# Performance work log

Hardware: AMD Instinct MI355X
Metric: run time of the kernel (lower is better)

The kernel has to match this reference:

```python
import jax, jax.numpy as jnp
import numpy as np

THRESHOLD = 0.0025
EPS = 1e-12
NORM_EPS = 1e-12  # torch F.normalize default eps


def _l2n(x):
    # F.normalize(x, p=2, dim=1): x / max(||x||_2, eps)
    n = jnp.sqrt(jnp.sum(x * x, axis=1, keepdims=True))
    return x / jnp.maximum(n, NORM_EPS)


def _memory_unit(feature, memory):
    # feature: [N, C], memory: [M, C]
    nf = _l2n(feature)
    nm = _l2n(memory)
    w = jax.nn.softmax(nf @ nm.T, axis=1)            # [N, M] cosine sims -> softmax
    # hard_shrink: relu(w - t) * w / (|w - t| + eps)
    w = jax.nn.relu(w - THRESHOLD) * w / (jnp.abs(w - THRESHOLD) + EPS)
    # L1 normalize rows
    w = w / jnp.maximum(jnp.sum(jnp.abs(w), axis=1, keepdims=True), NORM_EPS)
    mf = w @ memory                                   # [N, C] memory read
    return mf, w


def setup_inputs() -> dict:
    key = jax.random.key(0)
    ks = jax.random.split(key, 6)
    N, M = 16384, 1024
    chans = [256, 512, 1024]
    d = {}
    for i, c in enumerate(chans):
        d[f"feat{i}"] = jax.random.normal(ks[i], (N, c), dtype=jnp.float32)
        d[f"mem{i}"] = jax.random.normal(ks[3 + i], (M, c), dtype=jnp.float32)
    return d


def reference(feat0, feat1, feat2, mem0, mem1, mem2):
    outs = []
    weights = []
    for f, m in ((feat0, mem0), (feat1, mem1), (feat2, mem2)):
        mf, w = _memory_unit(f, m)
        outs.append(jnp.concatenate((mf, f), axis=1))  # cat along channel dim
        weights.append(w)
    return (outs[0], outs[1], outs[2], weights[0], weights[1], weights[2])
```

## Files before the change

### kernel.cpp

```cpp
#include <hip/hip_runtime.h>
#include <stdint.h>

typedef float f32x4 __attribute__((ext_vector_type(4)));
typedef short s16x8 __attribute__((ext_vector_type(8)));
typedef short s16x4 __attribute__((ext_vector_type(4)));

__device__ __forceinline__ unsigned short f2bf(float f) {
    uint32_t u = __float_as_uint(f);
    u += 0x7FFFu + ((u >> 16) & 1u);
    return (unsigned short)(u >> 16);
}

__device__ __forceinline__ void g2l16(const short* g, short* l) {
    __builtin_amdgcn_global_load_lds(
        (const __attribute__((address_space(1))) uint32_t*)g,
        (__attribute__((address_space(3))) uint32_t*)l, 16, 0, 0);
}

template<int C>
__device__ __forceinline__ void prep_body(const float* __restrict__ mp,
                                          short* __restrict__ nmp,
                                          int ct, short* stage) {
    const int tid = threadIdx.x;
    const int row = tid >> 4;
    const int c4  = tid & 15;
    constexpr int IT = C / 64;
    const f32x4* src = (const f32x4*)(mp + (size_t)(ct * 16 + row) * C);
    f32x4 vals[IT];
    float ss = 0.f;
#pragma unroll
    for (int i = 0; i < IT; ++i) {
        f32x4 v = src[c4 + 16 * i];
        vals[i] = v;
        ss += v.x * v.x + v.y * v.y + v.z * v.z + v.w * v.w;
    }
#pragma unroll
    for (int m = 1; m < 16; m <<= 1) ss += __shfl_xor(ss, m);
    const float inv = 1.f / fmaxf(sqrtf(ss), 1e-12f);
#pragma unroll
    for (int i = 0; i < IT; ++i) {
        f32x4 v = vals[i];
        s16x4 o;
        o[0] = (short)f2bf(v.x * inv);
        o[1] = (short)f2bf(v.y * inv);
        o[2] = (short)f2bf(v.z * inv);
        o[3] = (short)f2bf(v.w * inv);
        *(s16x4*)&stage[row * C + (c4 + 16 * i) * 4] = o;
    }
    __syncthreads();
    const int lane = tid & 63;
    const int wv = tid >> 6;
    constexpr int NKB = C / 32;
#pragma unroll
    for (int j = 0; j < NKB / 4; ++j) {
        const int kb = j * 4 + wv;
        const s16x8 v = *(const s16x8*)&stage[(lane & 15) * C + kb * 32 + (lane >> 4) * 8];
        *(s16x8*)&nmp[((size_t)ct * NKB + kb) * 512 + lane * 8] = v;
    }
}

__global__ __launch_bounds__(256) void prep_all(const float* m0, short* n0,
                                                const float* m1, short* n1,
                                                const float* m2, short* n2) {
    __shared__ short stage[16 * 1024];
    const int bid = blockIdx.x;
    if (bid < 64) prep_body<256>(m0, n0, bid, stage);
    else if (bid < 128) prep_body<512>(m1, n1, bid - 64, stage);
    else prep_body<1024>(m2, n2, bid - 128, stage);
}

template<int C>
__device__ __forceinline__ void gemm_body(const float* __restrict__ feat,
                                          const float* __restrict__ memv,
                                          const short* __restrict__ nm,
                                          float* __restrict__ out_cat,
                                          float* __restrict__ out_w,
                                          int tile,
                                          short* __restrict__ Bst,
                                          short* __restrict__ As,
                                          float (*__restrict__ red)[64],
                                          float* __restrict__ rowT,
                                          float* __restrict__ rowL,
                                          float* __restrict__ invL,
                                          int* __restrict__ rowflag,
                                          int* __restrict__ anyflag) {
    constexpr int NKB = C / 32;
    constexpr int NCH = C / 64;
    const int tid  = threadIdx.x;
    const int w    = tid >> 6;
    const int lane = tid & 63;
    const int g    = lane >> 4;
    const int ml   = lane & 15;
    const int swz  = ml & 7;
    const int row0 = tile * 64;

    const int frow = tid >> 4;
    const int fk4  = tid & 15;
    const float* fsrc = feat + (size_t)(row0 + frow) * C + fk4 * 4;
    const int ldsW = frow * 64 + (((fk4 >> 1) ^ (frow & 7)) << 3) + (fk4 & 1) * 4;
    const short* nbG = nm + (size_t)(w * 4) * NKB * 512 + lane * 8;
    short* bD0 = Bst + (w * 4) * 512 + lane * 8;
    short* bD1 = Bst + 32768 + (w * 4) * 512 + lane * 8;

    if (tid == 0) *anyflag = 0;

    f32x4 acc[4][4];
#pragma unroll
    for (int r = 0; r < 4; ++r)
#pragma unroll
        for (int ct = 0; ct < 4; ++ct)
            acc[r][ct] = (f32x4){0.f, 0.f, 0.f, 0.f};

    float ss = 0.f;

    const f32x4 v0 = *(const f32x4*)fsrc;
    f32x4 fnxt;
    if (NCH > 1) fnxt = *(const f32x4*)(fsrc + 64);
    __builtin_amdgcn_sched_barrier(0);
#pragma unroll
    for (int p = 0; p < 4; ++p)
        g2l16(nbG + (size_t)p * NKB * 512, bD0 + p * 512);
#pragma unroll
    for (int p = 0; p < 4; ++p)
        g2l16(nbG + ((size_t)p * NKB + 1) * 512, bD1 + p * 512);
    __builtin_amdgcn_sched_barrier(0);
    {
        ss += v0.x * v0.x + v0.y * v0.y + v0.z * v0.z + v0.w * v0.w;
        s16x4 o;
        o[0] = (short)f2bf(v0.x); o[1] = (short)f2bf(v0.y);
        o[2] = (short)f2bf(v0.z); o[3] = (short)f2bf(v0.w);
        *(s16x4*)&As[ldsW] = o;
    }
    asm volatile("s_waitcnt lgkmcnt(0)" ::: "memory");
    __builtin_amdgcn_s_barrier();
    asm volatile("" ::: "memory");

    for (int kb = 0; kb < NKB; ++kb) {
        const int chunk = kb >> 1;
        if ((kb & 1) == 0 && chunk + 1 < NCH) {
            ss += fnxt.x * fnxt.x + fnxt.y * fnxt.y + fnxt.z * fnxt.z + fnxt.w * fnxt.w;
            s16x4 o;
            o[0] = (short)f2bf(fnxt.x); o[1] = (short)f2bf(fnxt.y);
            o[2] = (short)f2bf(fnxt.z); o[3] = (short)f2bf(fnxt.w);
            *(s16x4*)&As[((chunk + 1) & 1) * 4096 + ldsW] = o;
        }
        if (kb == 0 || kb == NKB - 2) asm volatile("s_waitcnt vmcnt(4)" ::: "memory");
        else if (kb == NKB - 1)       asm volatile("s_waitcnt vmcnt(0)" ::: "memory");
        else                          asm volatile("s_waitcnt vmcnt(5)" ::: "memory");
        const short* Bb = Bst + (kb & 1) * 32768 + (w * 4) * 512 + lane * 8;
        s16x8 b[4];
#pragma unroll
        for (int p = 0; p < 4; ++p)
            b[p] = *(const s16x8*)(Bb + p * 512);
        const short* Ab = &As[(chunk & 1) * 4096];
        const int gr = ((kb & 1) << 2) | g;
        s16x8 a[4];
#pragma unroll
        for (int r = 0; r < 4; ++r)
            a[r] = *(const s16x8*)&Ab[(r * 16 + ml) * 64 + ((gr ^ swz) << 3)];
        asm volatile("s_waitcnt lgkmcnt(0)" ::: "memory");
        __builtin_amdgcn_sched_barrier(0);
        if (kb + 2 < NKB) {
            short* bDn = Bst + (kb & 1) * 32768 + (w * 4) * 512 + lane * 8;
#pragma unroll
            for (int p = 0; p < 4; ++p)
                g2l16(nbG + ((size_t)p * NKB + kb + 2) * 512, bDn + p * 512);
        }
        __builtin_amdgcn_sched_barrier(0);
        if ((kb & 1) == 0 && chunk + 2 < NCH)
            fnxt = *(const f32x4*)(fsrc + (size_t)(chunk + 2) * 64);
        __builtin_amdgcn_sched_barrier(0);
        __builtin_amdgcn_s_setprio(1);
#pragma unroll
        for (int r = 0; r < 4; ++r)
#pragma unroll
            for (int ct = 0; ct < 4; ++ct)
                acc[r][ct] = __builtin_amdgcn_mfma_f32_16x16x32_bf16(a[r], b[ct], acc[r][ct], 0, 0, 0);
        __builtin_amdgcn_s_setprio(0);
        if ((kb & 1) == 1 && kb + 1 < NKB) {
            asm volatile("s_waitcnt lgkmcnt(0)" ::: "memory");
            __builtin_amdgcn_s_barrier();
            asm volatile("" ::: "memory");
        }
    }

#pragma unroll
    for (int m = 1; m < 16; m <<= 1) ss += __shfl_xor(ss, m);
    if (fk4 == 0) invL[frow] = 1.f / fmaxf(sqrtf(ss), 1e-12f);
    __syncthreads();

#pragma unroll
    for (int r = 0; r < 4; ++r)
#pragma unroll
        for (int i = 0; i < 4; ++i) {
            const float inv = invL[r * 16 + 4 * g + i];
            float s = 0.f;
#pragma unroll
            for (int ct = 0; ct < 4; ++ct) {
                const float e = __expf(acc[r][ct][i] * inv);
                acc[r][ct][i] = e;
                s += e;
            }
#pragma unroll
            for (int m = 1; m < 16; m <<= 1) s += __shfl_xor(s, m);
            if (ml == 0) red[w][r * 16 + 4 * g + i] = s;
        }
    __syncthreads();
    if (tid < 64) {
        float t = red[0][tid];
#pragma unroll
        for (int ww = 1; ww < 16; ++ww) t += red[ww][tid];
        rowT[tid] = 1.f / t;
    }
    __syncthreads();

#pragma unroll
    for (int r = 0; r < 4; ++r)
#pragma unroll
        for (int i = 0; i < 4; ++i) {
            const float tinv = rowT[r * 16 + 4 * g + i];
            float l1 = 0.f;
#pragma unroll
            for (int ct = 0; ct < 4; ++ct) {
                const float wv = acc[r][ct][i] * tinv;
                const float d = wv - 0.0025f;
                const float v = (d > 0.f) ? (d * wv / (d + 1e-12f)) : 0.f;
                acc[r][ct][i] = v;
                l1 += v;
            }
#pragma unroll
            for (int m = 1; m < 16; m <<= 1) l1 += __shfl_xor(l1, m);
            if (ml == 0) red[w][r * 16 + 4 * g + i] = l1;
        }
    __syncthreads();
    if (tid < 64) {
        float t = red[0][tid];
#pragma unroll
        for (int ww = 1; ww < 16; ++ww) t += red[ww][tid];
        rowL[tid] = 1.f / fmaxf(t, 1e-12f);
        rowflag[tid] = (t > 0.f) ? 1 : 0;
        if (t > 0.f) *anyflag = 1;
    }
    __syncthreads();

#pragma unroll
    for (int r = 0; r < 4; ++r)
#pragma unroll
        for (int i = 0; i < 4; ++i) {
            const float il = rowL[r * 16 + 4 * g + i];
            float* orow = out_w + (size_t)(row0 + r * 16 + 4 * g + i) * 1024;
#pragma unroll
            for (int ct = 0; ct < 4; ++ct)
                orow[(w * 4 + ct) * 16 + ml] = acc[r][ct][i] * il;
        }

    {
        float* fzro = out_cat + (size_t)(row0 + frow) * (2 * C) + fk4 * 4;
        float* fcpy = out_cat + (size_t)(row0 + frow) * (2 * C) + C + fk4 * 4;
        const f32x4 z4 = {0.f, 0.f, 0.f, 0.f};
#pragma unroll
        for (int ch = 0; ch < NCH; ++ch)
            __builtin_nontemporal_store(z4, (f32x4*)(fzro + (size_t)ch * 64));
#pragma unroll
        for (int ch = 0; ch < NCH; ++ch) {
            const f32x4 v = *(const f32x4*)(fsrc + (size_t)ch * 64);
            __builtin_nontemporal_store(v, (f32x4*)(fcpy + (size_t)ch * 64));
        }
    }

    if (*anyflag != 0) {
        __threadfence();
        __syncthreads();
        constexpr int CC = C / 64;
#pragma unroll
        for (int rr = 0; rr < 4; ++rr) {
            const int row = w * 4 + rr;
            if (!rowflag[row]) continue;
            float* dst = out_cat + (size_t)(row0 + row) * (2 * C);
            float mfacc[CC];
#pragma unroll
            for (int cc = 0; cc < CC; ++cc) mfacc[cc] = 0.f;
            const float* wrow = out_w + (size_t)(row0 + row) * 1024;
            for (int jb = 0; jb < 1024; jb += 64) {
                const float wv = wrow[jb + lane];
                unsigned long long msk = __ballot(wv != 0.f);
                while (msk) {
                    const int j = __builtin_ctzll(msk);
                    msk &= msk - 1;
                    const float val = __shfl(wv, j);
                    const float* mrow = memv + (size_t)(jb + j) * C;
#pragma unroll
                    for (int cc = 0; cc < CC; ++cc)
                        mfacc[cc] += val * mrow[cc * 64 + lane];
                }
            }
#pragma unroll
            for (int cc = 0; cc < CC; ++cc) dst[cc * 64 + lane] = mfacc[cc];
        }
    }
}

__global__ __launch_bounds__(1024) void gemm_all(
        const float* f0, const float* m0, const short* n0, float* o0, float* w0,
        const float* f1, const float* m1, const short* n1, float* o1, float* w1,
        const float* f2, const float* m2, const short* n2, float* o2, float* w2) {
    __shared__ short Bst[2 * 32768];
    __shared__ short As[2 * 4096];
    __shared__ float red[16][64];
    __shared__ float rowT[64];
    __shared__ float rowL[64];
    __shared__ float invL[64];
    __shared__ int rowflag[64];
    __shared__ int anyflag;

    const int bid = blockIdx.x;
    if (bid < 256)
        gemm_body<1024>(f2, m2, n2, o2, w2, bid,
                        Bst, As, red, rowT, rowL, invL, rowflag, &anyflag);
    else if (bid < 512)
        gemm_body<512>(f1, m1, n1, o1, w1, bid - 256,
                       Bst, As, red, rowT, rowL, invL, rowflag, &anyflag);
    else
        gemm_body<256>(f0, m0, n0, o0, w0, bid - 512,
                       Bst, As, red, rowT, rowL, invL, rowflag, &anyflag);
}

extern "C" void kernel_launch(void* const* d_in, const int* in_sizes, int n_in,
                              void* d_out, int out_size, void* d_ws, size_t ws_size,
                              hipStream_t stream) {
    const float* feat[3] = {nullptr, nullptr, nullptr};
    const float* memp[3] = {nullptr, nullptr, nullptr};
    for (int i = 0; i < n_in && i < 6; ++i) {
        const int s = in_sizes[i];
        const float* p = (const float*)d_in[i];
        if (s == 16384 * 256) feat[0] = p;
        else if (s == 16384 * 512) feat[1] = p;
        else if (s == 16384 * 1024) feat[2] = p;
        else if (s == 1024 * 256) memp[0] = p;
        else if (s == 1024 * 512) memp[1] = p;
        else if (s == 1024 * 1024) memp[2] = p;
    }
    float* out = (float*)d_out;
    short* nm0 = (short*)d_ws;
    short* nm1 = nm0 + 1024 * 256;
    short* nm2 = nm1 + 1024 * 512;

    const size_t O0 = 0;
    const size_t O1 = (size_t)16384 * 512;
    const size_t O2 = O1 + (size_t)16384 * 1024;
    const size_t W0 = O2 + (size_t)16384 * 2048;
    const size_t W1 = W0 + (size_t)16384 * 1024;
    const size_t W2 = W1 + (size_t)16384 * 1024;

    prep_all<<<192, 256, 0, stream>>>(memp[0], nm0, memp[1], nm1, memp[2], nm2);

    gemm_all<<<768, 1024, 0, stream>>>(
        feat[0], memp[0], nm0, out + O0, out + W0,
        feat[1], memp[1], nm1, out + O1, out + W1,
        feat[2], memp[2], nm2, out + O2, out + W2);
}
```

Baseline: 174.5 us.

## Interleave feature copy and zero-fill stores into the GEMM main loop

Moves the copy of the input features into the concatenated output, and the zero-fill of the memory-feature half, out of the epilogue and into the K-loop. The stores reuse the feature values already loaded for bf16 conversion, so the second global read of the features goes away. The vmcnt wait counts are retuned to account for the extra in-flight stores. This risks mis-synchronisation if the counts are wrong. It also drops the nontemporal hint on these stores.

```diff
diff --git a/kernel.cpp b/kernel.cpp
--- a/kernel.cpp
+++ b/kernel.cpp
@@ -97,6 +97,9 @@
     const int frow = tid >> 4;
     const int fk4  = tid & 15;
     const float* fsrc = feat + (size_t)(row0 + frow) * C + fk4 * 4;
+    float* fcpy = out_cat + (size_t)(row0 + frow) * (2 * C) + C + fk4 * 4;
+    float* fzro = out_cat + (size_t)(row0 + frow) * (2 * C) + fk4 * 4;
+    const f32x4 z4 = {0.f, 0.f, 0.f, 0.f};
     const int ldsW = frow * 64 + (((fk4 >> 1) ^ (frow & 7)) << 3) + (fk4 & 1) * 4;
     const short* nbG = nm + (size_t)(w * 4) * NKB * 512 + lane * 8;
     short* bD0 = Bst + (w * 4) * 512 + lane * 8;
@@ -130,6 +133,7 @@
         o[0] = (short)f2bf(v0.x); o[1] = (short)f2bf(v0.y);
         o[2] = (short)f2bf(v0.z); o[3] = (short)f2bf(v0.w);
         *(s16x4*)&As[ldsW] = o;
+        *(f32x4*)fcpy = v0;
     }
     asm volatile("s_waitcnt lgkmcnt(0)" ::: "memory");
     __builtin_amdgcn_s_barrier();
@@ -137,16 +141,21 @@
 
     for (int kb = 0; kb < NKB; ++kb) {
         const int chunk = kb >> 1;
-        if ((kb & 1) == 0 && chunk + 1 < NCH) {
-            ss += fnxt.x * fnxt.x + fnxt.y * fnxt.y + fnxt.z * fnxt.z + fnxt.w * fnxt.w;
+        f32x4 fold;
+        const bool dofill = ((kb & 1) == 0 && chunk + 1 < NCH);
+        if (dofill) {
+            fold = fnxt;
+            ss += fold.x * fold.x + fold.y * fold.y + fold.z * fold.z + fold.w * fold.w;
             s16x4 o;
-            o[0] = (short)f2bf(fnxt.x); o[1] = (short)f2bf(fnxt.y);
-            o[2] = (short)f2bf(fnxt.z); o[3] = (short)f2bf(fnxt.w);
+            o[0] = (short)f2bf(fold.x); o[1] = (short)f2bf(fold.y);
+            o[2] = (short)f2bf(fold.z); o[3] = (short)f2bf(fold.w);
             *(s16x4*)&As[((chunk + 1) & 1) * 4096 + ldsW] = o;
         }
-        if (kb == 0 || kb == NKB - 2) asm volatile("s_waitcnt vmcnt(4)" ::: "memory");
-        else if (kb == NKB - 1)       asm volatile("s_waitcnt vmcnt(0)" ::: "memory");
-        else                          asm volatile("s_waitcnt vmcnt(5)" ::: "memory");
+        if (kb == 0)                 asm volatile("s_waitcnt vmcnt(5)" ::: "memory");
+        else if (kb == NKB - 1)      asm volatile("s_waitcnt vmcnt(2)" ::: "memory");
+        else if (kb == NKB - 3)      asm volatile("s_waitcnt vmcnt(6)" ::: "memory");
+        else if (kb & 1)             asm volatile("s_waitcnt vmcnt(7)" ::: "memory");
+        else                         asm volatile("s_waitcnt vmcnt(6)" ::: "memory");
         const short* Bb = Bst + (kb & 1) * 32768 + (w * 4) * 512 + lane * 8;
         s16x8 b[4];
 #pragma unroll
@@ -177,6 +186,15 @@
             for (int ct = 0; ct < 4; ++ct)
                 acc[r][ct] = __builtin_amdgcn_mfma_f32_16x16x32_bf16(a[r], b[ct], acc[r][ct], 0, 0, 0);
         __builtin_amdgcn_s_setprio(0);
+        __builtin_amdgcn_sched_barrier(0);
+        if (kb & 1) {
+            *(f32x4*)(fzro + (size_t)chunk * 64) = z4;
+        } else if (dofill) {
+            *(f32x4*)(fcpy + (size_t)(chunk + 1) * 64) = fold;
+        } else {
+            *(f32x4*)(fzro + (size_t)(NCH - 1) * 64) = z4;
+        }
+        __builtin_amdgcn_sched_barrier(0);
         if ((kb & 1) == 1 && kb + 1 < NKB) {
             asm volatile("s_waitcnt lgkmcnt(0)" ::: "memory");
             __builtin_amdgcn_s_barrier();
@@ -253,20 +271,6 @@
             for (int ct = 0; ct < 4; ++ct)
                 orow[(w * 4 + ct) * 16 + ml] = acc[r][ct][i] * il;
         }
-
-    {
-        float* fzro = out_cat + (size_t)(row0 + frow) * (2 * C) + fk4 * 4;
-        float* fcpy = out_cat + (size_t)(row0 + frow) * (2 * C) + C + fk4 * 4;
-        const f32x4 z4 = {0.f, 0.f, 0.f, 0.f};
-#pragma unroll
-        for (int ch = 0; ch < NCH; ++ch)
-            __builtin_nontemporal_store(z4, (f32x4*)(fzro + (size_t)ch * 64));
-#pragma unroll
-        for (int ch = 0; ch < NCH; ++ch) {
-            const f32x4 v = *(const f32x4*)(fsrc + (size_t)ch * 64);
-            __builtin_nontemporal_store(v, (f32x4*)(fcpy + (size_t)ch * 64));
-        }
-    }
 
     if (*anyflag != 0) {
         __threadfence();
```

New measurement: 202.0 us. 15.7% more time.
